# Performance work log

Measured on AMD Instinct MI355X. Metric: run time of the kernel, lower is better.

The kernel has to match this reference:

```python
import jax, jax.numpy as jnp
import numpy as np

A, B, C, D, DT, STEPS = 0.02, 0.2, -65.0, 8.0, 1.0, 100
H, I, O = 8192, 4096, 4096


def _compress(x, gain):
    return jnp.sign(x) * jnp.log1p(gain * jnp.abs(x) + 1e-6)


def setup_inputs() -> dict:
    key = jax.random.key(0)
    k1, k2, k3, k4, k5 = jax.random.split(key, 5)
    return {
        "v_input": jax.random.normal(k1, (I,), jnp.float32),
        "target_output": jax.random.normal(k2, (O,), jnp.float32),
        "W1": jax.random.uniform(k3, (H, I), jnp.float32) * 0.05,
        "W2": jax.random.uniform(k4, (O, H), jnp.float32) * 0.05,
        "W_feedback": jax.random.uniform(k5, (H, O), jnp.float32) * 0.02,
        "gain1": jnp.float32(1.0),
        "gain2": jnp.float32(1.0),
    }


def reference(v_input, target_output, W1, W2, W_feedback, gain1, gain2):
    # Input currents are loop-invariant in the original torch loop; compute once.
    I_hidden = _compress(W1 @ v_input, gain1)            # [H]
    I_output = _compress(W2 @ I_hidden, gain2)           # [O]
    I_hidden = I_hidden - W_feedback @ I_output          # [H]
    total_input = jnp.concatenate([I_hidden, I_output])  # [H+O]

    n = total_input.shape[0]
    v0 = jnp.full((n,), -65.0, jnp.float32)
    u0 = B * v0

    def step(carry, _):
        v_prev, u_prev = carry
        v = v_prev + DT * (0.04 * v_prev ** 2 + 5.0 * v_prev + 0.14 - u_prev + total_input)
        u = u_prev + DT * A * (B * v_prev - u_prev)
        spiked = v >= 30.0
        v = jnp.where(spiked, C, v)
        u = jnp.where(spiked, u + D, u)
        return (v, u), (v, u)

    _, (vs, us) = jax.lax.scan(step, (v0, u0), None, length=STEPS - 1)
    v_vec = jnp.concatenate([v0[None, :], vs], axis=0)  # [STEPS, H+O]
    u_vec = jnp.concatenate([u0[None, :], us], axis=0)

    loss = jnp.mean((I_output - target_output) ** 2)
    return loss, v_vec, u_vec
```

## Files before the change

### kernel.cpp

```cpp
#include <hip/hip_runtime.h>
#include <math.h>

#define HSZ 8192
#define ISZ 4096
#define OSZ 4096
#define NTOT (HSZ + OSZ)
#define STEPS 100

typedef unsigned short ushort8v __attribute__((ext_vector_type(8)));

__device__ __forceinline__ float bf2f(unsigned short h) {
    union { unsigned u; float f; } c; c.u = ((unsigned)h) << 16; return c.f;
}

__device__ __forceinline__ double compress_d(double x, double gain) {
    double s = (x > 0.0) ? 1.0 : ((x < 0.0) ? -1.0 : 0.0);
    return s * log1p(gain * fabs(x) + 1e-6);
}

__device__ __forceinline__ double wred(double a) {
    #pragma unroll
    for (int o = 32; o > 0; o >>= 1) a += __shfl_down(a, o, 64);
    return a;
}

__device__ __forceinline__ int detect_bf(const void* W1) {
    const unsigned short* p = (const unsigned short*)W1;
    const int lane = threadIdx.x & 63;
    const unsigned short a0 = (unsigned short)(p[lane] & 0x7FFF);
    const unsigned short a1 = (unsigned short)(p[64 + lane] & 0x7FFF);
    unsigned long long bad = __ballot((a0 > 0x3D80) || (a1 > 0x3D80));
    return bad == 0ull;
}

template <int K, int XIN, int DOCOMP>
__global__ __launch_bounds__(256) void mv_kernel(
        const void* __restrict__ W, const void* __restrict__ x,
        const void* __restrict__ gain, const float* __restrict__ base,
        float* __restrict__ y, const void* __restrict__ Wdet) {
    const int bf = detect_bf(Wdet);
    const int row = blockIdx.x;
    const int t = threadIdx.x;
    double acc = 0.0;
    if (bf) {
        const ushort8v* Wr = (const ushort8v*)((const unsigned short*)W + (size_t)row * K);
        if (XIN) {
            const ushort8v* xv = (const ushort8v*)x;
            #pragma unroll
            for (int c = 0; c < K / 2048; ++c) {
                const int i = c * 256 + t;
                ushort8v w = Wr[i], xx = xv[i];
                #pragma unroll
                for (int j = 0; j < 8; ++j)
                    acc += (double)bf2f(w[j]) * (double)bf2f(xx[j]);
            }
        } else {
            const float4* xv = (const float4*)x;
            #pragma unroll
            for (int c = 0; c < K / 2048; ++c) {
                const int i = c * 256 + t;
                ushort8v w = Wr[i];
                float4 x0 = xv[2 * i], x1 = xv[2 * i + 1];
                acc += (double)bf2f(w[0]) * (double)x0.x;
                acc += (double)bf2f(w[1]) * (double)x0.y;
                acc += (double)bf2f(w[2]) * (double)x0.z;
                acc += (double)bf2f(w[3]) * (double)x0.w;
                acc += (double)bf2f(w[4]) * (double)x1.x;
                acc += (double)bf2f(w[5]) * (double)x1.y;
                acc += (double)bf2f(w[6]) * (double)x1.z;
                acc += (double)bf2f(w[7]) * (double)x1.w;
            }
        }
    } else {
        const float4* Wr = (const float4*)((const float*)W + (size_t)row * K);
        const float4* xv = (const float4*)x;
        #pragma unroll
        for (int c = 0; c < K / 1024; ++c) {
            const int i = c * 256 + t;
            float4 w = Wr[i], xx = xv[i];
            acc += (double)w.x * (double)xx.x;
            acc += (double)w.y * (double)xx.y;
            acc += (double)w.z * (double)xx.z;
            acc += (double)w.w * (double)xx.w;
        }
    }
    acc = wred(acc);
    __shared__ double red[4];
    if ((t & 63) == 0) red[t >> 6] = acc;
    __syncthreads();
    if (t == 0) {
        const double s = red[0] + red[1] + red[2] + red[3];
        if (DOCOMP) {
            const float g = bf ? bf2f(*(const unsigned short*)gain) : *(const float*)gain;
            y[row] = (float)compress_d(s, (double)g);
        } else {
            y[row] = base[row] - (float)s;
        }
    }
}

__global__ __launch_bounds__(256) void sim_loss_kernel(
        const float* __restrict__ hid, const float* __restrict__ io,
        const void* __restrict__ tgt, float* __restrict__ loss_out,
        float* __restrict__ vout, float* __restrict__ uout,
        const void* __restrict__ Wdet) {
    if (blockIdx.x == NTOT / 256) {
        const int bf = detect_bf(Wdet);
        __shared__ double red[4];
        double acc = 0.0;
        for (int i = threadIdx.x; i < OSZ; i += 256) {
            const float tv = bf ? bf2f(((const unsigned short*)tgt)[i])
                                : ((const float*)tgt)[i];
            const double d = (double)io[i] - (double)tv;
            acc += d * d;
        }
        acc = wred(acc);
        if ((threadIdx.x & 63) == 0) red[threadIdx.x >> 6] = acc;
        __syncthreads();
        if (threadIdx.x == 0)
            loss_out[0] = (float)((red[0] + red[1] + red[2] + red[3]) / (double)OSZ);
        return;
    }
    const int n = blockIdx.x * 256 + threadIdx.x;
    const float ti = (n < HSZ) ? hid[n] : io[n - HSZ];
    float v = -65.0f;
    float u = -13.0f;
    vout[n] = v;
    uout[n] = u;
    for (int s = 1; s < STEPS; ++s) {
        float dv = 0.04f * (v * v);
        dv = dv + 5.0f * v;
        dv = dv + 0.14f;
        dv = dv - u;
        dv = dv + ti;
        float vn = v + 1.0f * dv;
        float du = 0.2f * v - u;
        float un = u + 0.02f * du;
        bool sp = (vn >= 30.0f);
        v = sp ? -65.0f : vn;
        u = sp ? (un + 8.0f) : un;
        vout[(size_t)s * NTOT + n] = v;
        uout[(size_t)s * NTOT + n] = u;
    }
}

extern "C" void kernel_launch(void* const* d_in, const int* in_sizes, int n_in,
                              void* d_out, int out_size, void* d_ws, size_t ws_size,
                              hipStream_t stream) {
    const void* v_input = d_in[0];
    const void* target  = d_in[1];
    const void* W1      = d_in[2];
    const void* W2      = d_in[3];
    const void* Wfb     = d_in[4];
    const void* gain1   = d_in[5];
    const void* gain2   = d_in[6];

    float* out  = (float*)d_out;
    float* vout = out + 1;
    float* uout = out + 1 + (size_t)STEPS * NTOT;

    float* h1c = (float*)d_ws;
    float* io  = h1c + HSZ;
    float* hid = io + OSZ;

    mv_kernel<ISZ, 1, 1><<<HSZ, 256, 0, stream>>>(W1, v_input, gain1, nullptr, h1c, W1);
    mv_kernel<HSZ, 0, 1><<<OSZ, 256, 0, stream>>>(W2, h1c, gain2, nullptr, io, W1);
    mv_kernel<OSZ, 0, 0><<<HSZ, 256, 0, stream>>>(Wfb, io, nullptr, h1c, hid, W1);
    sim_loss_kernel<<<NTOT / 256 + 1, 256, 0, stream>>>(hid, io, target, out, vout, uout, W1);
}
```

Before: 364.9 us.

## Fuse matvec chain and neuron simulation into one cooperative persistent kernel

```diff
diff --git a/kernel.cpp b/kernel.cpp
--- a/kernel.cpp
+++ b/kernel.cpp
@@ -1,5 +1,8 @@
 #include <hip/hip_runtime.h>
+#include <hip/hip_cooperative_groups.h>
 #include <math.h>
+
+namespace cg = cooperative_groups;
 
 #define HSZ 8192
 #define ISZ 4096
@@ -32,6 +35,140 @@
     unsigned long long bad = __ballot((a0 > 0x3D80) || (a1 > 0x3D80));
     return bad == 0ull;
 }
+
+template <int K, int XIN>
+__device__ __forceinline__ double wave_dot(const void* __restrict__ W,
+                                           const void* __restrict__ x,
+                                           int row, int lane, int bf) {
+    double acc = 0.0;
+    if (bf) {
+        const ushort8v* Wr = (const ushort8v*)((const unsigned short*)W + (size_t)row * K);
+        constexpr int NC = K / 512;
+        if (XIN) {
+            const ushort8v* xv = (const ushort8v*)x;
+            #pragma unroll 8
+            for (int c = 0; c < NC; ++c) {
+                const int i = c * 64 + lane;
+                ushort8v w = Wr[i], xx = xv[i];
+                #pragma unroll
+                for (int j = 0; j < 8; ++j)
+                    acc += (double)bf2f(w[j]) * (double)bf2f(xx[j]);
+            }
+        } else {
+            const float4* xv = (const float4*)x;
+            #pragma unroll 8
+            for (int c = 0; c < NC; ++c) {
+                const int i = c * 64 + lane;
+                ushort8v w = Wr[i];
+                float4 x0 = xv[2 * i], x1 = xv[2 * i + 1];
+                acc += (double)bf2f(w[0]) * (double)x0.x;
+                acc += (double)bf2f(w[1]) * (double)x0.y;
+                acc += (double)bf2f(w[2]) * (double)x0.z;
+                acc += (double)bf2f(w[3]) * (double)x0.w;
+                acc += (double)bf2f(w[4]) * (double)x1.x;
+                acc += (double)bf2f(w[5]) * (double)x1.y;
+                acc += (double)bf2f(w[6]) * (double)x1.z;
+                acc += (double)bf2f(w[7]) * (double)x1.w;
+            }
+        }
+    } else {
+        const float4* Wr = (const float4*)((const float*)W + (size_t)row * K);
+        const float4* xv = (const float4*)x;
+        constexpr int NC = K / 256;
+        #pragma unroll 8
+        for (int c = 0; c < NC; ++c) {
+            const int i = c * 64 + lane;
+            float4 w = Wr[i], xx = xv[i];
+            acc += (double)w.x * (double)xx.x;
+            acc += (double)w.y * (double)xx.y;
+            acc += (double)w.z * (double)xx.z;
+            acc += (double)w.w * (double)xx.w;
+        }
+    }
+    return wred(acc);
+}
+
+__global__ __launch_bounds__(256, 4) void fused_kernel(
+        const void* __restrict__ v_input, const void* __restrict__ target,
+        const void* __restrict__ W1, const void* __restrict__ W2,
+        const void* __restrict__ Wfb,
+        const void* __restrict__ gain1, const void* __restrict__ gain2,
+        float* __restrict__ h1c, float* __restrict__ io, float* __restrict__ hid,
+        float* __restrict__ loss_out, float* __restrict__ vout,
+        float* __restrict__ uout) {
+    cg::grid_group grid = cg::this_grid();
+    const int lane = threadIdx.x & 63;
+    const int wave = threadIdx.x >> 6;
+    const int gwid = blockIdx.x * 4 + wave;
+    const int gwaves = gridDim.x * 4;
+    const int bf = detect_bf(W1);
+
+    for (int row = gwid; row < HSZ; row += gwaves) {
+        double d = wave_dot<ISZ, 1>(W1, v_input, row, lane, bf);
+        if (lane == 0) {
+            const float g = bf ? bf2f(*(const unsigned short*)gain1)
+                               : *(const float*)gain1;
+            h1c[row] = (float)compress_d(d, (double)g);
+        }
+    }
+    grid.sync();
+
+    for (int row = gwid; row < OSZ; row += gwaves) {
+        double d = wave_dot<HSZ, 0>(W2, h1c, row, lane, bf);
+        if (lane == 0) {
+            const float g = bf ? bf2f(*(const unsigned short*)gain2)
+                               : *(const float*)gain2;
+            io[row] = (float)compress_d(d, (double)g);
+        }
+    }
+    grid.sync();
+
+    for (int row = gwid; row < HSZ; row += gwaves) {
+        double d = wave_dot<OSZ, 0>(Wfb, io, row, lane, bf);
+        if (lane == 0) hid[row] = h1c[row] - (float)d;
+    }
+    grid.sync();
+
+    if (blockIdx.x == gridDim.x - 1) {
+        __shared__ double red[4];
+        double acc = 0.0;
+        for (int i = threadIdx.x; i < OSZ; i += 256) {
+            const float tv = bf ? bf2f(((const unsigned short*)target)[i])
+                                : ((const float*)target)[i];
+            const double dd = (double)io[i] - (double)tv;
+            acc += dd * dd;
+        }
+        acc = wred(acc);
+        if ((threadIdx.x & 63) == 0) red[threadIdx.x >> 6] = acc;
+        __syncthreads();
+        if (threadIdx.x == 0)
+            loss_out[0] = (float)((red[0] + red[1] + red[2] + red[3]) / (double)OSZ);
+    }
+    const int tid = blockIdx.x * 256 + threadIdx.x;
+    for (int n = tid; n < NTOT; n += gridDim.x * 256) {
+        const float ti = (n < HSZ) ? hid[n] : io[n - HSZ];
+        float v = -65.0f;
+        float u = -13.0f;
+        vout[n] = v;
+        uout[n] = u;
+        for (int s = 1; s < STEPS; ++s) {
+            float dv = 0.04f * (v * v);
+            dv = dv + 5.0f * v;
+            dv = dv + 0.14f;
+            dv = dv - u;
+            dv = dv + ti;
+            float vn = v + 1.0f * dv;
+            float du = 0.2f * v - u;
+            float un = u + 0.02f * du;
+            bool sp = (vn >= 30.0f);
+            v = sp ? -65.0f : vn;
+            u = sp ? (un + 8.0f) : un;
+            vout[(size_t)s * NTOT + n] = v;
+            uout[(size_t)s * NTOT + n] = u;
+        }
+    }
+}
+
 
 template <int K, int XIN, int DOCOMP>
 __global__ __launch_bounds__(256) void mv_kernel(
@@ -163,6 +300,36 @@
     float* io  = h1c + HSZ;
     float* hid = io + OSZ;
 
+    static int coop_blocks = -2;
+    if (coop_blocks == -2) {
+        int per_cu = 0, num_cu = 256, dev = 0;
+        hipGetDevice(&dev);
+        hipDeviceProp_t prop;
+        if (hipGetDeviceProperties(&prop, dev) == hipSuccess && prop.multiProcessorCount > 0)
+            num_cu = prop.multiProcessorCount;
+        hipError_t e = hipOccupancyMaxActiveBlocksPerMultiprocessor(&per_cu, fused_kernel, 256, 0);
+        if (e != hipSuccess || per_cu <= 0) {
+            coop_blocks = -1;
+        } else {
+            long b = (long)per_cu * num_cu;
+            if (b > 2048) b = 2048;
+            coop_blocks = (int)b;
+        }
+    }
+
+    if (coop_blocks > 0) {
+        void* args[] = {
+            (void*)&v_input, (void*)&target, (void*)&W1, (void*)&W2, (void*)&Wfb,
+            (void*)&gain1, (void*)&gain2,
+            (void*)&h1c, (void*)&io, (void*)&hid,
+            (void*)&out, (void*)&vout, (void*)&uout,
+        };
+        hipError_t e = hipLaunchCooperativeKernel(fused_kernel, dim3(coop_blocks),
+                                                  dim3(256), args, 0, stream);
+        if (e == hipSuccess) return;
+        coop_blocks = -1;
+    }
+
     mv_kernel<ISZ, 1, 1><<<HSZ, 256, 0, stream>>>(W1, v_input, gain1, nullptr, h1c, W1);
     mv_kernel<HSZ, 0, 1><<<OSZ, 256, 0, stream>>>(W2, h1c, gain2, nullptr, io, W1);
     mv_kernel<OSZ, 0, 0><<<HSZ, 256, 0, stream>>>(Wfb, io, nullptr, h1c, hid, W1);
```

New measurement: 651.9 us. +78.7%, slower.
